# Kernel optimization log

Measured on AMD Instinct MI355X. Metric: run time of the kernel, lower is better.

## Reference

```python
import jax, jax.numpy as jnp
import numpy as np
from jax import lax

B, T, D, H = 256, 512, 128, 256  # batch, seq_len, input_dim, hidden_dim


def _lstm_layer(x_seq, Wih, Whh, bih, bhh):
    """Single PyTorch-convention LSTM layer. x_seq: [B,T,Din] -> [B,T,H].
    Gate order i, f, g, o; h0 = c0 = 0."""
    Bsz = x_seq.shape[0]
    Hd = Whh.shape[1]
    # Precompute input contributions for all timesteps: [B,T,4H]
    xg = jnp.einsum('btd,gd->btg', x_seq, Wih) + bih + bhh

    def step(carry, xg_t):
        h, c = carry
        gates = xg_t + h @ Whh.T  # [B,4H]
        i, f, g, o = jnp.split(gates, 4, axis=-1)
        i = jax.nn.sigmoid(i)
        f = jax.nn.sigmoid(f)
        g = jnp.tanh(g)
        o = jax.nn.sigmoid(o)
        c = f * c + i * g
        h = o * jnp.tanh(c)
        return (h, c), h

    init = (jnp.zeros((Bsz, Hd), x_seq.dtype), jnp.zeros((Bsz, Hd), x_seq.dtype))
    _, hs = lax.scan(step, init, jnp.swapaxes(xg, 0, 1))  # hs: [T,B,H]
    return jnp.swapaxes(hs, 0, 1)


def setup_inputs() -> dict:
    key = jax.random.key(0)
    ks = jax.random.split(key, 12)
    x = jax.random.normal(ks[0], (B, T, D), dtype=jnp.float32)
    # Left-contiguous mask: lengths in [1, T] (pack_padded_sequence semantics)
    lengths = jax.random.randint(ks[1], (B,), 1, T + 1)
    mask = (jnp.arange(T)[None, :] < lengths[:, None]).astype(jnp.int32)
    s0 = 1.0 / np.sqrt(H)
    u = lambda k, shape: jax.random.uniform(k, shape, jnp.float32, -s0, s0)
    return {
        'x': x,
        'mask': mask,
        'W_ih0': u(ks[2], (4 * H, D)),
        'W_hh0': u(ks[3], (4 * H, H)),
        'b_ih0': u(ks[4], (4 * H,)),
        'b_hh0': u(ks[5], (4 * H,)),
        'W_ih1': u(ks[6], (4 * H, H)),
        'W_hh1': u(ks[7], (4 * H, H)),
        'b_ih1': u(ks[8], (4 * H,)),
        'b_hh1': u(ks[9], (4 * H,)),
        'fc_w': u(ks[10], (1, H)),
        'fc_b': u(ks[11], (1,)),
    }


def reference(x, mask, W_ih0, W_hh0, b_ih0, b_hh0, W_ih1, W_hh1, b_ih1, b_hh1, fc_w, fc_b):
    # 2-layer LSTM (dropout inactive at inference)
    h1 = _lstm_layer(x, W_ih0, W_hh0, b_ih0, b_hh0)   # [B,T,H]
    h2 = _lstm_layer(h1, W_ih1, W_hh1, b_ih1, b_hh1)  # [B,T,H]
    # Gather output at last valid timestep per sequence (== packed result)
    lens = jnp.sum(mask, axis=1)                      # [B]
    last = h2[jnp.arange(h2.shape[0]), lens - 1]      # [B,H]
    return last @ fc_w.T + fc_b                       # [B,1]
```

## Files before the change

kernel.cpp:

```cpp
#include <hip/hip_runtime.h>
#include <stdint.h>

#define B_ 256
#define T_ 512
#define D_ 128
#define H_ 256

typedef __attribute__((ext_vector_type(8))) _Float16 half8;
typedef __attribute__((ext_vector_type(4))) float f32x4;
typedef __attribute__((ext_vector_type(4))) int i32x4;

#define WS_PART 0
#define WS_H0   65536
#define WS_H1   (65536 + 2*B_*H_*4)

__device__ __forceinline__ float fast_sig(float x) {
    return 1.0f / (1.0f + __expf(-x));
}
__device__ __forceinline__ float fast_tanh(float x) {
    float xc = fminf(fmaxf(x, -30.0f), 30.0f);
    float e = __expf(-2.0f * xc);
    return (1.0f - e) / (1.0f + e);
}
__device__ __forceinline__ half8 cvt8(const float* p) {
    const f32x4* q = (const f32x4*)p;
    f32x4 a = q[0], b = q[1];
    half8 r;
    r[0] = (_Float16)a[0]; r[1] = (_Float16)a[1];
    r[2] = (_Float16)a[2]; r[3] = (_Float16)a[3];
    r[4] = (_Float16)b[0]; r[5] = (_Float16)b[1];
    r[6] = (_Float16)b[2]; r[7] = (_Float16)b[3];
    return r;
}

__device__ __forceinline__ void poll8(const unsigned* p0, const unsigned* p1, i32x4* r) {
    asm volatile(
        "global_load_dwordx4 %0, %8, off sc0 sc1\n\t"
        "global_load_dwordx4 %1, %8, off offset:16 sc0 sc1\n\t"
        "global_load_dwordx4 %2, %8, off offset:128 sc0 sc1\n\t"
        "global_load_dwordx4 %3, %8, off offset:144 sc0 sc1\n\t"
        "global_load_dwordx4 %4, %9, off sc0 sc1\n\t"
        "global_load_dwordx4 %5, %9, off offset:16 sc0 sc1\n\t"
        "global_load_dwordx4 %6, %9, off offset:128 sc0 sc1\n\t"
        "global_load_dwordx4 %7, %9, off offset:144 sc0 sc1\n\t"
        "s_waitcnt vmcnt(0)"
        : "=&v"(r[0]), "=&v"(r[1]), "=&v"(r[2]), "=&v"(r[3]),
          "=&v"(r[4]), "=&v"(r[5]), "=&v"(r[6]), "=&v"(r[7])
        : "v"(p0), "v"(p1) : "memory");
}
__device__ __forceinline__ void store_dw_mall(unsigned* p, unsigned v) {
    asm volatile("global_store_dword %0, %1, off sc0 sc1" :: "v"(p), "v"(v) : "memory");
}

__global__ __launch_bounds__(256, 1) void lstm_main(
    const float* __restrict__ x, const int* __restrict__ mask,
    const float* __restrict__ Wih0, const float* __restrict__ Whh0,
    const float* __restrict__ bih0, const float* __restrict__ bhh0,
    const float* __restrict__ Wih1, const float* __restrict__ Whh1,
    const float* __restrict__ bih1, const float* __restrict__ bhh1,
    const float* __restrict__ fcw, char* __restrict__ ws)
{
    const int tid  = threadIdx.x;
    const int blk  = blockIdx.x;
    const int g    = blk & 15;
    const int sl   = blk >> 4;
    const int b0   = g * 16;
    const int j0   = sl * 16;
    const int w    = tid >> 6;
    const int lane = tid & 63;
    const int row  = lane & 15;
    const int quad = lane >> 4;
    const int kb   = quad * 8;

    float*    partials = (float*)(ws + WS_PART);
    unsigned* h0u      = (unsigned*)(ws + WS_H0);
    unsigned* h1u      = (unsigned*)(ws + WS_H1);

    __shared__ float gbuf[2048];
    __shared__ __align__(16) _Float16 hsh0[16 * 264];
    __shared__ __align__(16) _Float16 hsh1[16 * 264];

    const int n = w * H_ + j0 + row;
    half8 wA[12], wB[16];
#pragma unroll
    for (int kt = 0; kt < 4; ++kt) wA[kt]     = cvt8(&Wih0[(size_t)n * D_ + kt * 32 + kb]);
#pragma unroll
    for (int kt = 0; kt < 8; ++kt) wA[4 + kt] = cvt8(&Whh0[(size_t)n * H_ + kt * 32 + kb]);
#pragma unroll
    for (int kt = 0; kt < 8; ++kt) wB[kt]     = cvt8(&Wih1[(size_t)n * H_ + kt * 32 + kb]);
#pragma unroll
    for (int kt = 0; kt < 8; ++kt) wB[8 + kt] = cvt8(&Whh1[(size_t)n * H_ + kt * 32 + kb]);
    const float biasA = bih0[n] + bhh0[n];
    const float biasB = bih1[n] + bhh1[n];

    const int bb    = tid >> 4;
    const int jj    = tid & 15;
    const int bglob = b0 + bb;

    int len = 0;
    {
        const int* mrow = mask + (size_t)bglob * T_ + jj * 32;
#pragma unroll
        for (int q = 0; q < 32; ++q) len += mrow[q];
#pragma unroll
        for (int o = 1; o < 16; o <<= 1) len += __shfl_xor(len, o, 16);
    }

    float c0 = 0.f, c1 = 0.f, hsave = 0.f;

    const float* xrow = x + (size_t)(b0 + row) * T_ * D_ + kb;
    f32x4 xacc = {0.f, 0.f, 0.f, 0.f};
#pragma unroll
    for (int kt = 0; kt < 4; ++kt)
        xacc = __builtin_amdgcn_mfma_f32_16x16x32_f16(cvt8(xrow + kt * 32), wA[kt], xacc, 0, 0, 0);

    for (int u = 0; u <= T_; ++u) {
        half8 a0[8], a1[8];

        if (u >= 1) {
            const unsigned tag0 = (unsigned)u << 16;
            const unsigned tag1 = (u >= 2) ? ((unsigned)(u - 1) << 16) : tag0;
            const unsigned* p0 = h0u + ((size_t)((u - 1) & 1) * B_ + (b0 + row)) * H_ + w * 64 + quad * 8;
            const unsigned* p1 = (u >= 2)
                ? h1u + ((size_t)(u & 1) * B_ + (b0 + row)) * H_ + w * 64 + quad * 8
                : p0;
            i32x4 r[8];
            int guard = 0;
            while (true) {
                poll8(p0, p1, r);
                unsigned m = 0;
#pragma unroll
                for (int i = 0; i < 4; ++i) {
                    m |= ((unsigned)r[i][0] ^ tag0); m |= ((unsigned)r[i][1] ^ tag0);
                    m |= ((unsigned)r[i][2] ^ tag0); m |= ((unsigned)r[i][3] ^ tag0);
                }
#pragma unroll
                for (int i = 4; i < 8; ++i) {
                    m |= ((unsigned)r[i][0] ^ tag1); m |= ((unsigned)r[i][1] ^ tag1);
                    m |= ((unsigned)r[i][2] ^ tag1); m |= ((unsigned)r[i][3] ^ tag1);
                }
                if (__all((m & 0xFFFF0000u) == 0)) break;
                if (++guard > (1 << 15)) break;
            }
#pragma unroll
            for (int t = 0; t < 2; ++t) {
                i32x4 pk;
                pk[0] = (r[2 * t][0] & 0xFFFF) | (r[2 * t][1] << 16);
                pk[1] = (r[2 * t][2] & 0xFFFF) | (r[2 * t][3] << 16);
                pk[2] = (r[2 * t + 1][0] & 0xFFFF) | (r[2 * t + 1][1] << 16);
                pk[3] = (r[2 * t + 1][2] & 0xFFFF) | (r[2 * t + 1][3] << 16);
                *(i32x4*)(hsh0 + row * 264 + w * 64 + t * 32 + quad * 8) = pk;
            }
            if (u >= 2) {
#pragma unroll
                for (int t = 0; t < 2; ++t) {
                    i32x4 pk;
                    pk[0] = (r[4 + 2 * t][0] & 0xFFFF) | (r[4 + 2 * t][1] << 16);
                    pk[1] = (r[4 + 2 * t][2] & 0xFFFF) | (r[4 + 2 * t][3] << 16);
                    pk[2] = (r[5 + 2 * t][0] & 0xFFFF) | (r[5 + 2 * t][1] << 16);
                    pk[3] = (r[5 + 2 * t][2] & 0xFFFF) | (r[5 + 2 * t][3] << 16);
                    *(i32x4*)(hsh1 + row * 264 + w * 64 + t * 32 + quad * 8) = pk;
                }
            }
            __syncthreads();
#pragma unroll
            for (int kt = 0; kt < 8; ++kt)
                a0[kt] = *(const half8*)(hsh0 + row * 264 + kt * 32 + quad * 8);
            if (u >= 2) {
#pragma unroll
                for (int kt = 0; kt < 8; ++kt)
                    a1[kt] = *(const half8*)(hsh1 + row * 264 + kt * 32 + quad * 8);
            }
        }

        f32x4 acc0 = xacc;
        f32x4 acc1 = {0.f, 0.f, 0.f, 0.f};
        if (u >= 1) {
#pragma unroll
            for (int kt = 0; kt < 8; ++kt) {
                if (u < T_) acc0 = __builtin_amdgcn_mfma_f32_16x16x32_f16(a0[kt], wA[4 + kt], acc0, 0, 0, 0);
                acc1 = __builtin_amdgcn_mfma_f32_16x16x32_f16(a0[kt], wB[kt], acc1, 0, 0, 0);
            }
            if (u >= 2) {
#pragma unroll
                for (int kt = 0; kt < 8; ++kt)
                    acc1 = __builtin_amdgcn_mfma_f32_16x16x32_f16(a1[kt], wB[8 + kt], acc1, 0, 0, 0);
            }
        }

        if (u < T_) {
#pragma unroll
            for (int r = 0; r < 4; ++r)
                gbuf[w * 256 + (quad * 4 + r) * 16 + row] = acc0[r] + biasA;
        }
        if (u >= 1) {
#pragma unroll
            for (int r = 0; r < 4; ++r)
                gbuf[1024 + w * 256 + (quad * 4 + r) * 16 + row] = acc1[r] + biasB;
        }
        __syncthreads();

        const int idx = bb * 16 + jj;
        if (u < T_) {
            float gi = fast_sig(gbuf[idx]);
            float gf = fast_sig(gbuf[256 + idx]);
            float gg = fast_tanh(gbuf[512 + idx]);
            float go = fast_sig(gbuf[768 + idx]);
            c0 = gf * c0 + gi * gg;
            float h0v = go * fast_tanh(c0);
            union { _Float16 h; unsigned short s; } cv; cv.h = (_Float16)h0v;
            store_dw_mall(h0u + ((size_t)(u & 1) * B_ + bglob) * H_ + j0 + jj,
                          ((unsigned)(u + 1) << 16) | cv.s);
        }
        if (u >= 1) {
            float gi = fast_sig(gbuf[1024 + idx]);
            float gf = fast_sig(gbuf[1024 + 256 + idx]);
            float gg = fast_tanh(gbuf[1024 + 512 + idx]);
            float go = fast_sig(gbuf[1024 + 768 + idx]);
            c1 = gf * c1 + gi * gg;
            float h1v = go * fast_tanh(c1);
            union { _Float16 h; unsigned short s; } cv; cv.h = (_Float16)h1v;
            store_dw_mall(h1u + ((size_t)((u - 1) & 1) * B_ + bglob) * H_ + j0 + jj,
                          ((unsigned)u << 16) | cv.s);
            if (u == len) hsave = h1v;
        }

        if (u < T_ - 1) {
            const float* xp = xrow + (size_t)(u + 1) * D_;
            f32x4 t = {0.f, 0.f, 0.f, 0.f};
#pragma unroll
            for (int kt = 0; kt < 4; ++kt)
                t = __builtin_amdgcn_mfma_f32_16x16x32_f16(cvt8(xp + kt * 32), wA[kt], t, 0, 0, 0);
            xacc = t;
        }
    }

    float part = hsave * fcw[j0 + jj];
#pragma unroll
    for (int o = 1; o < 16; o <<= 1) part += __shfl_xor(part, o, 16);
    if (jj == 0) partials[sl * B_ + bglob] = part;
}

__global__ void lstm_fc(const float* __restrict__ fcb, const char* __restrict__ ws,
                        float* __restrict__ out) {
    const int b = threadIdx.x;
    const float* partials = (const float*)(ws + WS_PART);
    float s = fcb[0];
#pragma unroll
    for (int sl = 0; sl < 16; ++sl) s += partials[sl * B_ + b];
    out[b] = s;
}

extern "C" void kernel_launch(void* const* d_in, const int* in_sizes, int n_in,
                              void* d_out, int out_size, void* d_ws, size_t ws_size,
                              hipStream_t stream) {
    const float* xx    = (const float*)d_in[0];
    const int*   mask  = (const int*)d_in[1];
    const float* Wih0  = (const float*)d_in[2];
    const float* Whh0  = (const float*)d_in[3];
    const float* bih0  = (const float*)d_in[4];
    const float* bhh0  = (const float*)d_in[5];
    const float* Wih1  = (const float*)d_in[6];
    const float* Whh1  = (const float*)d_in[7];
    const float* bih1  = (const float*)d_in[8];
    const float* bhh1  = (const float*)d_in[9];
    const float* fcw   = (const float*)d_in[10];
    const float* fcb   = (const float*)d_in[11];

    lstm_main<<<dim3(256), dim3(256), 0, stream>>>(
        xx, mask, Wih0, Whh0, bih0, bhh0, Wih1, Whh1, bih1, bhh1, fcw, (char*)d_ws);
    lstm_fc<<<dim3(1), dim3(256), 0, stream>>>(fcb, (const char*)d_ws, (float*)d_out);
}
```

Measured before the change: 2.015 ms.

## Split layer-0 and layer-1 gate phases to publish h0 earlier, prefetch next x

Reorders each timestep so the layer-0 MFMAs, gate nonlinearities and h0 store finish before layer-1 work starts. Other blocks waiting on h0 can then proceed sooner along the critical recurrent chain. The next timestep's x row is now loaded at the top of the loop so its latency overlaps the spin-wait. The gate buffer rows are padded from 16 to 18 floats to reduce LDS bank conflicts. This adds a second __syncthreads per step and raises register pressure for the prefetched x values.

```diff
diff --git a/kernel.cpp b/kernel.cpp
--- a/kernel.cpp
+++ b/kernel.cpp
@@ -25,6 +25,14 @@
 __device__ __forceinline__ half8 cvt8(const float* p) {
     const f32x4* q = (const f32x4*)p;
     f32x4 a = q[0], b = q[1];
+    half8 r;
+    r[0] = (_Float16)a[0]; r[1] = (_Float16)a[1];
+    r[2] = (_Float16)a[2]; r[3] = (_Float16)a[3];
+    r[4] = (_Float16)b[0]; r[5] = (_Float16)b[1];
+    r[6] = (_Float16)b[2]; r[7] = (_Float16)b[3];
+    return r;
+}
+__device__ __forceinline__ half8 cvt8v(f32x4 a, f32x4 b) {
     half8 r;
     r[0] = (_Float16)a[0]; r[1] = (_Float16)a[1];
     r[2] = (_Float16)a[2]; r[3] = (_Float16)a[3];
@@ -51,6 +59,10 @@
 __device__ __forceinline__ void store_dw_mall(unsigned* p, unsigned v) {
     asm volatile("global_store_dword %0, %1, off sc0 sc1" :: "v"(p), "v"(v) : "memory");
 }
+
+#define GB_M  18
+#define GB_G  (16 * GB_M)
+#define GB_L  (4 * GB_G)
 
 __global__ __launch_bounds__(256, 1) void lstm_main(
     const float* __restrict__ x, const int* __restrict__ mask,
@@ -76,7 +88,7 @@
     unsigned* h0u      = (unsigned*)(ws + WS_H0);
     unsigned* h1u      = (unsigned*)(ws + WS_H1);
 
-    __shared__ float gbuf[2048];
+    __shared__ float gbuf[2 * GB_L];
     __shared__ __align__(16) _Float16 hsh0[16 * 264];
     __shared__ __align__(16) _Float16 hsh1[16 * 264];
 
@@ -115,8 +127,15 @@
         xacc = __builtin_amdgcn_mfma_f32_16x16x32_f16(cvt8(xrow + kt * 32), wA[kt], xacc, 0, 0, 0);
 
     for (int u = 0; u <= T_; ++u) {
+        f32x4 xr[8];
+        {
+            const int tn = (u + 1 < T_) ? (u + 1) : (T_ - 1);
+            const f32x4* q = (const f32x4*)(xrow + (size_t)tn * D_);
+#pragma unroll
+            for (int kt = 0; kt < 4; ++kt) { xr[2 * kt] = q[kt * 8]; xr[2 * kt + 1] = q[kt * 8 + 1]; }
+        }
+
         half8 a0[8], a1[8];
-
         if (u >= 1) {
             const unsigned tag0 = (unsigned)u << 16;
             const unsigned tag1 = (u >= 2) ? ((unsigned)(u - 1) << 16) : tag0;
@@ -173,50 +192,47 @@
             }
         }
 
-        f32x4 acc0 = xacc;
-        f32x4 acc1 = {0.f, 0.f, 0.f, 0.f};
-        if (u >= 1) {
-#pragma unroll
-            for (int kt = 0; kt < 8; ++kt) {
-                if (u < T_) acc0 = __builtin_amdgcn_mfma_f32_16x16x32_f16(a0[kt], wA[4 + kt], acc0, 0, 0, 0);
-                acc1 = __builtin_amdgcn_mfma_f32_16x16x32_f16(a0[kt], wB[kt], acc1, 0, 0, 0);
-            }
-            if (u >= 2) {
+        if (u < T_) {
+            f32x4 acc0 = xacc;
+            if (u >= 1) {
 #pragma unroll
                 for (int kt = 0; kt < 8; ++kt)
-                    acc1 = __builtin_amdgcn_mfma_f32_16x16x32_f16(a1[kt], wB[8 + kt], acc1, 0, 0, 0);
-            }
-        }
-
-        if (u < T_) {
+                    acc0 = __builtin_amdgcn_mfma_f32_16x16x32_f16(a0[kt], wA[4 + kt], acc0, 0, 0, 0);
+            }
 #pragma unroll
             for (int r = 0; r < 4; ++r)
-                gbuf[w * 256 + (quad * 4 + r) * 16 + row] = acc0[r] + biasA;
-        }
-        if (u >= 1) {
-#pragma unroll
-            for (int r = 0; r < 4; ++r)
-                gbuf[1024 + w * 256 + (quad * 4 + r) * 16 + row] = acc1[r] + biasB;
-        }
-        __syncthreads();
-
-        const int idx = bb * 16 + jj;
-        if (u < T_) {
-            float gi = fast_sig(gbuf[idx]);
-            float gf = fast_sig(gbuf[256 + idx]);
-            float gg = fast_tanh(gbuf[512 + idx]);
-            float go = fast_sig(gbuf[768 + idx]);
+                gbuf[w * GB_G + (quad * 4 + r) * GB_M + row] = acc0[r] + biasA;
+            __syncthreads();
+            float gi = fast_sig(gbuf[0 * GB_G + bb * GB_M + jj]);
+            float gf = fast_sig(gbuf[1 * GB_G + bb * GB_M + jj]);
+            float gg = fast_tanh(gbuf[2 * GB_G + bb * GB_M + jj]);
+            float go = fast_sig(gbuf[3 * GB_G + bb * GB_M + jj]);
             c0 = gf * c0 + gi * gg;
             float h0v = go * fast_tanh(c0);
             union { _Float16 h; unsigned short s; } cv; cv.h = (_Float16)h0v;
             store_dw_mall(h0u + ((size_t)(u & 1) * B_ + bglob) * H_ + j0 + jj,
                           ((unsigned)(u + 1) << 16) | cv.s);
         }
+        __builtin_amdgcn_sched_barrier(0);
+
         if (u >= 1) {
-            float gi = fast_sig(gbuf[1024 + idx]);
-            float gf = fast_sig(gbuf[1024 + 256 + idx]);
-            float gg = fast_tanh(gbuf[1024 + 512 + idx]);
-            float go = fast_sig(gbuf[1024 + 768 + idx]);
+            f32x4 acc1 = {0.f, 0.f, 0.f, 0.f};
+#pragma unroll
+            for (int kt = 0; kt < 8; ++kt)
+                acc1 = __builtin_amdgcn_mfma_f32_16x16x32_f16(a0[kt], wB[kt], acc1, 0, 0, 0);
+            if (u >= 2) {
+#pragma unroll
+                for (int kt = 0; kt < 8; ++kt)
+                    acc1 = __builtin_amdgcn_mfma_f32_16x16x32_f16(a1[kt], wB[8 + kt], acc1, 0, 0, 0);
+            }
+#pragma unroll
+            for (int r = 0; r < 4; ++r)
+                gbuf[GB_L + w * GB_G + (quad * 4 + r) * GB_M + row] = acc1[r] + biasB;
+            __syncthreads();
+            float gi = fast_sig(gbuf[GB_L + 0 * GB_G + bb * GB_M + jj]);
+            float gf = fast_sig(gbuf[GB_L + 1 * GB_G + bb * GB_M + jj]);
+            float gg = fast_tanh(gbuf[GB_L + 2 * GB_G + bb * GB_M + jj]);
+            float go = fast_sig(gbuf[GB_L + 3 * GB_G + bb * GB_M + jj]);
             c1 = gf * c1 + gi * gg;
             float h1v = go * fast_tanh(c1);
             union { _Float16 h; unsigned short s; } cv; cv.h = (_Float16)h1v;
@@ -226,11 +242,10 @@
         }
 
         if (u < T_ - 1) {
-            const float* xp = xrow + (size_t)(u + 1) * D_;
             f32x4 t = {0.f, 0.f, 0.f, 0.f};
 #pragma unroll
             for (int kt = 0; kt < 4; ++kt)
-                t = __builtin_amdgcn_mfma_f32_16x16x32_f16(cvt8(xp + kt * 32), wA[kt], t, 0, 0, 0);
+                t = __builtin_amdgcn_mfma_f32_16x16x32_f16(cvt8v(xr[2 * kt], xr[2 * kt + 1]), wA[kt], t, 0, 0, 0);
             xacc = t;
         }
     }
```

New measurement: 1.978 ms. About the same (-1.8%).

## Split layer polls, prefetch next-step h and x loads to overlap latency

Applied to the files above, without the earlier changes.

The single combined poll of both layers' hidden states is split so layer 0 waits only for its own h, runs its gates, and only then waits for layer 1's h. Speculative loads for the next step's h0/h1 are issued at the end of each iteration and checked at the start of the next, and the next x row is loaded early into registers. The aim is to hide global-memory polling latency and decouple the two layers' dependency chains. It adds extra __syncthreads per step and relies on inline-asm waitcnt tying to keep loads ordered correctly.

```diff
diff --git a/kernel.cpp b/kernel.cpp
--- a/kernel.cpp
+++ b/kernel.cpp
@@ -32,24 +32,62 @@
     r[6] = (_Float16)b[2]; r[7] = (_Float16)b[3];
     return r;
 }
-
-__device__ __forceinline__ void poll8(const unsigned* p0, const unsigned* p1, i32x4* r) {
+__device__ __forceinline__ half8 cvt8v(f32x4 a, f32x4 b) {
+    half8 r;
+    r[0] = (_Float16)a[0]; r[1] = (_Float16)a[1];
+    r[2] = (_Float16)a[2]; r[3] = (_Float16)a[3];
+    r[4] = (_Float16)b[0]; r[5] = (_Float16)b[1];
+    r[6] = (_Float16)b[2]; r[7] = (_Float16)b[3];
+    return r;
+}
+
+__device__ __forceinline__ void poll4_issue(const unsigned* p, i32x4* r) {
     asm volatile(
-        "global_load_dwordx4 %0, %8, off sc0 sc1\n\t"
-        "global_load_dwordx4 %1, %8, off offset:16 sc0 sc1\n\t"
-        "global_load_dwordx4 %2, %8, off offset:128 sc0 sc1\n\t"
-        "global_load_dwordx4 %3, %8, off offset:144 sc0 sc1\n\t"
-        "global_load_dwordx4 %4, %9, off sc0 sc1\n\t"
-        "global_load_dwordx4 %5, %9, off offset:16 sc0 sc1\n\t"
-        "global_load_dwordx4 %6, %9, off offset:128 sc0 sc1\n\t"
-        "global_load_dwordx4 %7, %9, off offset:144 sc0 sc1\n\t"
+        "global_load_dwordx4 %0, %4, off sc0 sc1\n\t"
+        "global_load_dwordx4 %1, %4, off offset:16 sc0 sc1\n\t"
+        "global_load_dwordx4 %2, %4, off offset:128 sc0 sc1\n\t"
+        "global_load_dwordx4 %3, %4, off offset:144 sc0 sc1"
+        : "=&v"(r[0]), "=&v"(r[1]), "=&v"(r[2]), "=&v"(r[3])
+        : "v"(p) : "memory");
+}
+__device__ __forceinline__ void poll4_wait(const unsigned* p, i32x4* r) {
+    asm volatile(
+        "global_load_dwordx4 %0, %4, off sc0 sc1\n\t"
+        "global_load_dwordx4 %1, %4, off offset:16 sc0 sc1\n\t"
+        "global_load_dwordx4 %2, %4, off offset:128 sc0 sc1\n\t"
+        "global_load_dwordx4 %3, %4, off offset:144 sc0 sc1\n\t"
         "s_waitcnt vmcnt(0)"
-        : "=&v"(r[0]), "=&v"(r[1]), "=&v"(r[2]), "=&v"(r[3]),
-          "=&v"(r[4]), "=&v"(r[5]), "=&v"(r[6]), "=&v"(r[7])
-        : "v"(p0), "v"(p1) : "memory");
+        : "=&v"(r[0]), "=&v"(r[1]), "=&v"(r[2]), "=&v"(r[3])
+        : "v"(p) : "memory");
+}
+__device__ __forceinline__ void wait_tie8(i32x4* a, i32x4* b) {
+    asm volatile("s_waitcnt vmcnt(0)"
+        : "+v"(a[0]), "+v"(a[1]), "+v"(a[2]), "+v"(a[3]),
+          "+v"(b[0]), "+v"(b[1]), "+v"(b[2]), "+v"(b[3]) :: "memory");
 }
 __device__ __forceinline__ void store_dw_mall(unsigned* p, unsigned v) {
     asm volatile("global_store_dword %0, %1, off sc0 sc1" :: "v"(p), "v"(v) : "memory");
+}
+
+__device__ __forceinline__ int tags_ok(const i32x4* r, unsigned tag) {
+    unsigned m = 0;
+#pragma unroll
+    for (int i = 0; i < 4; ++i) {
+        m |= ((unsigned)r[i][0] ^ tag); m |= ((unsigned)r[i][1] ^ tag);
+        m |= ((unsigned)r[i][2] ^ tag); m |= ((unsigned)r[i][3] ^ tag);
+    }
+    return __all((m & 0xFFFF0000u) == 0);
+}
+__device__ __forceinline__ void unpack_to_lds(const i32x4* r, _Float16* base) {
+#pragma unroll
+    for (int t = 0; t < 2; ++t) {
+        i32x4 pk;
+        pk[0] = (r[2 * t][0] & 0xFFFF) | (r[2 * t][1] << 16);
+        pk[1] = (r[2 * t][2] & 0xFFFF) | (r[2 * t][3] << 16);
+        pk[2] = (r[2 * t + 1][0] & 0xFFFF) | (r[2 * t + 1][1] << 16);
+        pk[3] = (r[2 * t + 1][2] & 0xFFFF) | (r[2 * t + 1][3] << 16);
+        *(i32x4*)(base + t * 32) = pk;
+    }
 }
 
 __global__ __launch_bounds__(256, 1) void lstm_main(
@@ -114,94 +152,54 @@
     for (int kt = 0; kt < 4; ++kt)
         xacc = __builtin_amdgcn_mfma_f32_16x16x32_f16(cvt8(xrow + kt * 32), wA[kt], xacc, 0, 0, 0);
 
+    i32x4 r0[4], r1[4];
+    const int koff = w * 64 + quad * 8;
+
     for (int u = 0; u <= T_; ++u) {
         half8 a0[8], a1[8];
+        f32x4 xr[8];
+        int h1ok = 1;
+        const unsigned tag1 = (unsigned)(u - 1) << 16;
 
         if (u >= 1) {
+            wait_tie8(r0, r1);
             const unsigned tag0 = (unsigned)u << 16;
-            const unsigned tag1 = (u >= 2) ? ((unsigned)(u - 1) << 16) : tag0;
-            const unsigned* p0 = h0u + ((size_t)((u - 1) & 1) * B_ + (b0 + row)) * H_ + w * 64 + quad * 8;
-            const unsigned* p1 = (u >= 2)
-                ? h1u + ((size_t)(u & 1) * B_ + (b0 + row)) * H_ + w * 64 + quad * 8
-                : p0;
-            i32x4 r[8];
+            const unsigned* p0 = h0u + ((size_t)((u - 1) & 1) * B_ + (b0 + row)) * H_ + koff;
             int guard = 0;
-            while (true) {
-                poll8(p0, p1, r);
-                unsigned m = 0;
-#pragma unroll
-                for (int i = 0; i < 4; ++i) {
-                    m |= ((unsigned)r[i][0] ^ tag0); m |= ((unsigned)r[i][1] ^ tag0);
-                    m |= ((unsigned)r[i][2] ^ tag0); m |= ((unsigned)r[i][3] ^ tag0);
-                }
-#pragma unroll
-                for (int i = 4; i < 8; ++i) {
-                    m |= ((unsigned)r[i][0] ^ tag1); m |= ((unsigned)r[i][1] ^ tag1);
-                    m |= ((unsigned)r[i][2] ^ tag1); m |= ((unsigned)r[i][3] ^ tag1);
-                }
-                if (__all((m & 0xFFFF0000u) == 0)) break;
+            while (!tags_ok(r0, tag0)) {
+                poll4_wait(p0, r0);
                 if (++guard > (1 << 15)) break;
             }
-#pragma unroll
-            for (int t = 0; t < 2; ++t) {
-                i32x4 pk;
-                pk[0] = (r[2 * t][0] & 0xFFFF) | (r[2 * t][1] << 16);
-                pk[1] = (r[2 * t][2] & 0xFFFF) | (r[2 * t][3] << 16);
-                pk[2] = (r[2 * t + 1][0] & 0xFFFF) | (r[2 * t + 1][1] << 16);
-                pk[3] = (r[2 * t + 1][2] & 0xFFFF) | (r[2 * t + 1][3] << 16);
-                *(i32x4*)(hsh0 + row * 264 + w * 64 + t * 32 + quad * 8) = pk;
+            h1ok = (u >= 2) ? tags_ok(r1, tag1) : 1;
+            {
+                const int tn = (u + 1 < T_) ? (u + 1) : (T_ - 1);
+                const f32x4* q = (const f32x4*)(xrow + (size_t)tn * D_);
+#pragma unroll
+                for (int kt = 0; kt < 4; ++kt) { xr[2 * kt] = q[kt * 8]; xr[2 * kt + 1] = q[kt * 8 + 1]; }
             }
-            if (u >= 2) {
-#pragma unroll
-                for (int t = 0; t < 2; ++t) {
-                    i32x4 pk;
-                    pk[0] = (r[4 + 2 * t][0] & 0xFFFF) | (r[4 + 2 * t][1] << 16);
-                    pk[1] = (r[4 + 2 * t][2] & 0xFFFF) | (r[4 + 2 * t][3] << 16);
-                    pk[2] = (r[5 + 2 * t][0] & 0xFFFF) | (r[5 + 2 * t][1] << 16);
-                    pk[3] = (r[5 + 2 * t][2] & 0xFFFF) | (r[5 + 2 * t][3] << 16);
-                    *(i32x4*)(hsh1 + row * 264 + w * 64 + t * 32 + quad * 8) = pk;
-                }
-            }
+            unpack_to_lds(r0, hsh0 + row * 264 + koff);
             __syncthreads();
 #pragma unroll
             for (int kt = 0; kt < 8; ++kt)
                 a0[kt] = *(const half8*)(hsh0 + row * 264 + kt * 32 + quad * 8);
-            if (u >= 2) {
+        } else {
+            const f32x4* q = (const f32x4*)(xrow + (size_t)1 * D_);
+#pragma unroll
+            for (int kt = 0; kt < 4; ++kt) { xr[2 * kt] = q[kt * 8]; xr[2 * kt + 1] = q[kt * 8 + 1]; }
+        }
+
+        if (u < T_) {
+            f32x4 acc0 = xacc;
+            if (u >= 1) {
 #pragma unroll
                 for (int kt = 0; kt < 8; ++kt)
-                    a1[kt] = *(const half8*)(hsh1 + row * 264 + kt * 32 + quad * 8);
+                    acc0 = __builtin_amdgcn_mfma_f32_16x16x32_f16(a0[kt], wA[4 + kt], acc0, 0, 0, 0);
             }
-        }
-
-        f32x4 acc0 = xacc;
-        f32x4 acc1 = {0.f, 0.f, 0.f, 0.f};
-        if (u >= 1) {
-#pragma unroll
-            for (int kt = 0; kt < 8; ++kt) {
-                if (u < T_) acc0 = __builtin_amdgcn_mfma_f32_16x16x32_f16(a0[kt], wA[4 + kt], acc0, 0, 0, 0);
-                acc1 = __builtin_amdgcn_mfma_f32_16x16x32_f16(a0[kt], wB[kt], acc1, 0, 0, 0);
-            }
-            if (u >= 2) {
-#pragma unroll
-                for (int kt = 0; kt < 8; ++kt)
-                    acc1 = __builtin_amdgcn_mfma_f32_16x16x32_f16(a1[kt], wB[8 + kt], acc1, 0, 0, 0);
-            }
-        }
-
-        if (u < T_) {
 #pragma unroll
             for (int r = 0; r < 4; ++r)
                 gbuf[w * 256 + (quad * 4 + r) * 16 + row] = acc0[r] + biasA;
-        }
-        if (u >= 1) {
-#pragma unroll
-            for (int r = 0; r < 4; ++r)
-                gbuf[1024 + w * 256 + (quad * 4 + r) * 16 + row] = acc1[r] + biasB;
-        }
-        __syncthreads();
-
-        const int idx = bb * 16 + jj;
-        if (u < T_) {
+            __syncthreads();
+            const int idx = bb * 16 + jj;
             float gi = fast_sig(gbuf[idx]);
             float gf = fast_sig(gbuf[256 + idx]);
             float gg = fast_tanh(gbuf[512 + idx]);
@@ -212,7 +210,35 @@
             store_dw_mall(h0u + ((size_t)(u & 1) * B_ + bglob) * H_ + j0 + jj,
                           ((unsigned)(u + 1) << 16) | cv.s);
         }
+        __builtin_amdgcn_sched_barrier(0);
+
         if (u >= 1) {
+            f32x4 acc1 = {0.f, 0.f, 0.f, 0.f};
+#pragma unroll
+            for (int kt = 0; kt < 8; ++kt)
+                acc1 = __builtin_amdgcn_mfma_f32_16x16x32_f16(a0[kt], wB[kt], acc1, 0, 0, 0);
+            if (u >= 2) {
+                const unsigned* p1 = h1u + ((size_t)(u & 1) * B_ + (b0 + row)) * H_ + koff;
+                int guard = 0;
+                while (!h1ok) {
+                    poll4_wait(p1, r1);
+                    h1ok = tags_ok(r1, tag1);
+                    if (++guard > (1 << 15)) break;
+                }
+                unpack_to_lds(r1, hsh1 + row * 264 + koff);
+                __syncthreads();
+#pragma unroll
+                for (int kt = 0; kt < 8; ++kt)
+                    a1[kt] = *(const half8*)(hsh1 + row * 264 + kt * 32 + quad * 8);
+#pragma unroll
+                for (int kt = 0; kt < 8; ++kt)
+                    acc1 = __builtin_amdgcn_mfma_f32_16x16x32_f16(a1[kt], wB[8 + kt], acc1, 0, 0, 0);
+            }
+#pragma unroll
+            for (int r = 0; r < 4; ++r)
+                gbuf[1024 + w * 256 + (quad * 4 + r) * 16 + row] = acc1[r] + biasB;
+            __syncthreads();
+            const int idx = bb * 16 + jj;
             float gi = fast_sig(gbuf[1024 + idx]);
             float gf = fast_sig(gbuf[1024 + 256 + idx]);
             float gg = fast_tanh(gbuf[1024 + 512 + idx]);
@@ -225,12 +251,21 @@
             if (u == len) hsave = h1v;
         }
 
+        if (u < T_) {
+            const int v = u + 1;
+            const unsigned* q0 = h0u + ((size_t)((v - 1) & 1) * B_ + (b0 + row)) * H_ + koff;
+            const unsigned* q1 = (v >= 2)
+                ? h1u + ((size_t)(v & 1) * B_ + (b0 + row)) * H_ + koff
+                : q0;
+            poll4_issue(q0, r0);
+            poll4_issue(q1, r1);
+        }
+
         if (u < T_ - 1) {
-            const float* xp = xrow + (size_t)(u + 1) * D_;
             f32x4 t = {0.f, 0.f, 0.f, 0.f};
 #pragma unroll
             for (int kt = 0; kt < 4; ++kt)
-                t = __builtin_amdgcn_mfma_f32_16x16x32_f16(cvt8(xp + kt * 32), wA[kt], t, 0, 0, 0);
+                t = __builtin_amdgcn_mfma_f32_16x16x32_f16(cvt8v(xr[2 * kt], xr[2 * kt + 1]), wA[kt], t, 0, 0, 0);
             xacc = t;
         }
     }
```

Measured after the change: 1.709 ms. 1.18x faster.
